# Kernel optimization log

Hardware: AMD Instinct MI355X
Metric: run time of the kernel (lower is better)

The kernel has to match this reference:

```python
import jax, jax.numpy as jnp
import numpy as np

D = 128        # embed_d
L = 2          # n_layers
B = 4096       # batch of center nodes (drugs)
S = 10         # num_samples per neighbor type (hard-coded in node_het_agg)
NUM_CELLS, NUM_DRUGS, NUM_GENES = 2000, 4000, 20000
DRUG_F, GENE_F = 1024, 2048
NT = 3         # node types: cell, drug, gene


def setup_inputs() -> dict:
    key = jax.random.key(0)
    ks = jax.random.split(key, 16)
    s = 0.02
    inp = {
        # raw per-type feature tables (feature_loader / embedding table)
        "drug_feats": jax.random.normal(ks[0], (NUM_DRUGS, DRUG_F), jnp.float32),
        "gene_feats": jax.random.normal(ks[1], (NUM_GENES, GENE_F), jnp.float32),
        "cell_tab": jax.random.normal(ks[2], (NUM_CELLS, D), jnp.float32) * s,
        # feat_proj linears
        "W_drug": jax.random.normal(ks[3], (DRUG_F, D), jnp.float32) * s,
        "b_drug": jnp.zeros((D,), jnp.float32),
        "W_gene": jax.random.normal(ks[4], (GENE_F, D), jnp.float32) * s,
        "b_gene": jnp.zeros((D,), jnp.float32),
        # RnnGnnLayer params: per layer, per neighbor type, a simple tanh RNN
        "rnn_Wx": jax.random.normal(ks[5], (L, NT, D, D), jnp.float32) * s,
        "rnn_Wh": jax.random.normal(ks[6], (L, NT, D, D), jnp.float32) * s,
        "rnn_b": jnp.zeros((L, NT, D), jnp.float32),
        # per-layer attention vector over [self || candidate]
        "att_w": jax.random.normal(ks[7], (L, 2 * D), jnp.float32) * s,
        # center node ids (drug type) and pre-sampled neighbor ids per layer/type
        "center_ids": jax.random.randint(ks[8], (B,), 0, NUM_DRUGS, jnp.int32),
        "cell_neigh": jax.random.randint(ks[9], (L, B, S), 0, NUM_CELLS, jnp.int32),
        "drug_neigh": jax.random.randint(ks[10], (L, B, S), 0, NUM_DRUGS, jnp.int32),
        "gene_neigh": jax.random.randint(ks[11], (L, B, S), 0, NUM_GENES, jnp.int32),
    }
    return inp


def reference(drug_feats, gene_feats, cell_tab, W_drug, b_drug, W_gene, b_gene,
              rnn_Wx, rnn_Wh, rnn_b, att_w,
              center_ids, cell_neigh, drug_neigh, gene_neigh):
    # conteng_agg per node type: gather raw features then project to embed_d
    def emb_cell(idx):
        return cell_tab[idx]                              # [..., D]

    def emb_drug(idx):
        return drug_feats[idx] @ W_drug + b_drug          # gather [..., DRUG_F] -> [..., D]

    def emb_gene(idx):
        return gene_feats[idx] @ W_gene + b_gene

    def rnn_agg(x, Wx, Wh, b):
        # x: [B, S, D]; simple tanh RNN over the S sampled neighbors, last hidden
        def step(h, xt):
            h = jnp.tanh(xt @ Wx + h @ Wh + b)
            return h, None
        h0 = jnp.zeros((x.shape[0], Wx.shape[1]), x.dtype)
        h_last, _ = jax.lax.scan(step, h0, jnp.swapaxes(x, 0, 1))
        return h_last                                      # [B, D]

    h = emb_drug(center_ids)                               # initial center embeds [B, D]
    n_layers = rnn_Wx.shape[0]
    for l in range(n_layers):
        neigh = [(cell_neigh[l], emb_cell), (drug_neigh[l], emb_drug), (gene_neigh[l], emb_gene)]
        aggs = []
        for t, (idx, emb) in enumerate(neigh):
            x = emb(idx)                                   # [B, S, D]
            aggs.append(rnn_agg(x, rnn_Wx[l, t], rnn_Wh[l, t], rnn_b[l, t]))
        cands = jnp.stack([h] + aggs, axis=1)              # [B, 1+NT, D]
        self_b = jnp.broadcast_to(h[:, None, :], cands.shape)
        scores = jax.nn.leaky_relu(jnp.concatenate([self_b, cands], axis=-1) @ att_w[l])  # [B, 1+NT]
        alpha = jax.nn.softmax(scores, axis=1)
        h = jnp.einsum('bc,bcd->bd', alpha, cands)         # attention-weighted combine
    return h                                               # [B, D]
```

## Files before the change

kernel.cpp:

```cpp
#include <hip/hip_runtime.h>
#include <stdint.h>

#define D 128
#define Ssz 10
#define HP 136
#define NB 4096

typedef uint16_t u16;
typedef uint32_t u32;
typedef __attribute__((ext_vector_type(8))) short short8;
typedef __attribute__((ext_vector_type(4))) float f32x4;

#define AS1U32(p) ((const __attribute__((address_space(1))) u32*)(p))
#define AS3U32(p) ((__attribute__((address_space(3))) u32*)(p))

__device__ __forceinline__ u16 f2bf(float f){
  u32 x = __float_as_uint(f);
  return (u16)((x + 0x7fffu + ((x >> 16) & 1u)) >> 16);
}
__device__ __forceinline__ float bf2f(u16 u){ return __uint_as_float(((u32)u) << 16); }

__device__ __forceinline__ float ftanh(float x){
  float e = __expf(2.0f * x);
  return 1.0f - 2.0f / (e + 1.0f);
}

__global__ __launch_bounds__(256) void prep_kernel(
    const float* __restrict__ W_drug, const float* __restrict__ W_gene,
    const float* __restrict__ rnn_Wx, const float* __restrict__ rnn_Wh,
    const float* __restrict__ cell_tab,
    u16* __restrict__ WdT, u16* __restrict__ WgT,
    u16* __restrict__ WxT6, u16* __restrict__ WhT6,
    u16* __restrict__ cellT)
{
  int i = blockIdx.x * 256 + threadIdx.x;
  if (i < 131072){
    int n = i >> 10, k = i & 1023;
    WdT[i] = f2bf(W_drug[k * D + n]);
  } else if (i < 393216){
    int j = i - 131072;
    int n = j >> 11, k = j & 2047;
    WgT[j] = f2bf(W_gene[k * D + n]);
  } else if (i < 491520){
    int j = i - 393216;
    int n = (j >> 7) & 127, k = j & 127;
    WxT6[j] = f2bf(rnn_Wx[(j & ~16383) + k * D + n]);
  } else if (i < 589824){
    int j = i - 491520;
    int n = (j >> 7) & 127, k = j & 127;
    WhT6[j] = f2bf(rnn_Wh[(j & ~16383) + k * D + n]);
  } else {
    int j = i - 589824;
    float v0 = cell_tab[2 * j], v1 = cell_tab[2 * j + 1];
    ((u32*)cellT)[j] = (u32)f2bf(v0) | ((u32)f2bf(v1) << 16);
  }
}

__global__ __launch_bounds__(256) void proj_gemm(
    const float* __restrict__ feats, int K, int M,
    const u16* __restrict__ WT,
    const float* __restrict__ bias,
    const u16* __restrict__ Wx0,
    const u16* __restrict__ Wx1,
    const float* __restrict__ rb0,
    const float* __restrict__ rb1,
    float* __restrict__ xw0,
    float* __restrict__ xw1,
    float* __restrict__ outf)
{
  __shared__ u16 Bt[128 * 128];

  int lane = threadIdx.x & 63;
  int wave = threadIdx.x >> 6;
  int quad = lane >> 4, l16 = lane & 15;
  int m0 = blockIdx.x * 64 + wave * 16;

  int row = min(m0 + l16, M - 1);
  const float* aptr = feats + (long)row * K + quad * 8;

  int st_nrow = wave * 32 + (lane >> 4);
  int st_p    = lane & 15;

  f32x4 acc[8];
#pragma unroll
  for (int nt = 0; nt < 8; ++nt){
    float bv = bias[nt * 16 + l16];
    f32x4 t = {bv, bv, bv, bv};
    acc[nt] = t;
  }

  f32x4 afA[4][2], afB[4][2];
#pragma unroll
  for (int ks = 0; ks < 4; ++ks){
    afA[ks][0] = *(const f32x4*)(aptr + ks * 32);
    afA[ks][1] = *(const f32x4*)(aptr + ks * 32 + 4);
  }

  auto chunk_step = [&](f32x4 (&acur)[4][2], f32x4 (&anxt)[4][2], int kc) {
#pragma unroll
    for (int j = 0; j < 8; ++j){
      int n = st_nrow + j * 4;
      int c = st_p ^ (n & 15);
      const u16* g = WT + (long)n * K + kc + c * 8;
      __builtin_amdgcn_global_load_lds(AS1U32(g),
                                       AS3U32(&Bt[(wave * 8 + j) * 512]),
                                       16, 0, 0);
    }
    if (kc + 128 < K){
#pragma unroll
      for (int ks = 0; ks < 4; ++ks){
        anxt[ks][0] = *(const f32x4*)(aptr + kc + 128 + ks * 32);
        anxt[ks][1] = *(const f32x4*)(aptr + kc + 128 + ks * 32 + 4);
      }
    }
    __syncthreads();

#pragma unroll
    for (int ks = 0; ks < 4; ++ks){
      short8 a;
#pragma unroll
      for (int q = 0; q < 4; ++q){
        a[q]     = (short)f2bf(acur[ks][0][q]);
        a[4 + q] = (short)f2bf(acur[ks][1][q]);
      }
#pragma unroll
      for (int nt = 0; nt < 8; ++nt){
        int n = nt * 16 + l16;
        int p = (ks * 4 + quad) ^ l16;
        short8 b = *(const short8*)(&Bt[n * 128 + p * 8]);
        acc[nt] = __builtin_amdgcn_mfma_f32_16x16x32_bf16(a, b, acc[nt], 0, 0, 0);
      }
    }
    __syncthreads();
  };

  for (int kc = 0; kc < K; kc += 256){
    chunk_step(afA, afB, kc);
    chunk_step(afB, afA, kc + 128);
  }

  if (outf){
#pragma unroll
    for (int nt = 0; nt < 8; ++nt){
      int col = nt * 16 + l16;
#pragma unroll
      for (int r = 0; r < 4; ++r){
        int mr = m0 + quad * 4 + r;
        if (mr < M) outf[(long)mr * D + col] = acc[nt][r];
      }
    }
  }

  u16* Pl = Bt + wave * 2176;
#pragma unroll
  for (int nt = 0; nt < 8; ++nt)
#pragma unroll
    for (int r = 0; r < 4; ++r)
      Pl[(quad * 4 + r) * HP + nt * 16 + l16] = f2bf(acc[nt][r]);
  __syncthreads();

  short8 paf[4];
#pragma unroll
  for (int ks = 0; ks < 4; ++ks)
    paf[ks] = *(const short8*)(&Pl[l16 * HP + ks * 32 + quad * 8]);

  auto xw_pass = [&](const u16* Wx, const float* rb, float* xw){
    f32x4 ac2[8];
#pragma unroll
    for (int nt = 0; nt < 8; ++nt){
      float bv = rb[nt * 16 + l16];
      f32x4 tv = {bv, bv, bv, bv};
      ac2[nt] = tv;
    }
#pragma unroll
    for (int nt = 0; nt < 8; ++nt){
#pragma unroll
      for (int ks = 0; ks < 4; ++ks){
        short8 b = *(const short8*)(Wx + (nt * 16 + l16) * D + ks * 32 + quad * 8);
        ac2[nt] = __builtin_amdgcn_mfma_f32_16x16x32_bf16(paf[ks], b, ac2[nt], 0, 0, 0);
      }
    }
#pragma unroll
    for (int nt = 0; nt < 8; ++nt){
      int col = nt * 16 + l16;
#pragma unroll
      for (int r = 0; r < 4; ++r){
        int mr = m0 + quad * 4 + r;
        if (mr < M) xw[(long)mr * D + col] = ac2[nt][r];
      }
    }
  };
  xw_pass(Wx0, rb0, xw0);
  xw_pass(Wx1, rb1, xw1);
}

__global__ __launch_bounds__(256) void xw_cell(
    const u16* __restrict__ cellT,
    const u16* __restrict__ WxT6,
    const float* __restrict__ bvec,
    float* __restrict__ xwb)
{
  int l = blockIdx.y;
  int mat = l * 3;
  const u16* WT = WxT6 + (size_t)mat * 16384;

  int lane = threadIdx.x & 63, wave = threadIdx.x >> 6;
  int quad = lane >> 4, l16 = lane & 15;
  int mt = blockIdx.x * 64 + wave * 16;
  int mr = min(mt + l16, 1999);

  short8 a[4];
#pragma unroll
  for (int ks = 0; ks < 4; ++ks)
    a[ks] = *(const short8*)(cellT + (long)mr * D + ks * 32 + quad * 8);

  f32x4 acc[8];
#pragma unroll
  for (int nt = 0; nt < 8; ++nt){
    float bv = bvec[mat * D + nt * 16 + l16];
    f32x4 tv = {bv, bv, bv, bv};
    acc[nt] = tv;
  }
#pragma unroll
  for (int nt = 0; nt < 8; ++nt){
#pragma unroll
    for (int ks = 0; ks < 4; ++ks){
      short8 b = *(const short8*)(WT + (nt * 16 + l16) * D + ks * 32 + quad * 8);
      acc[nt] = __builtin_amdgcn_mfma_f32_16x16x32_bf16(a[ks], b, acc[nt], 0, 0, 0);
    }
  }
#pragma unroll
  for (int nt = 0; nt < 8; ++nt){
    int col = nt * 16 + l16;
#pragma unroll
    for (int r = 0; r < 4; ++r){
      int mrow = mt + quad * 4 + r;
      if (mrow < 2000)
        xwb[((long)l * 26000 + mrow) * D + col] = acc[nt][r];
    }
  }
}

__global__ __launch_bounds__(256, 3) void rnn6_kernel(
    const float* __restrict__ xwb,
    const u16* __restrict__ WhT6,
    const int* __restrict__ cn, const int* __restrict__ dn,
    const int* __restrict__ gn,
    u16* __restrict__ agg)
{
  __shared__ u16 hbuf[16 * HP];

  int t = blockIdx.y, l = blockIdx.z;
  const int* idx = (t == 0) ? cn : (t == 1) ? dn : gn;
  int rbase = (t == 0) ? 0 : (t == 1) ? 2000 : 6000;
  int nmax  = (t == 0) ? 2000 : (t == 1) ? 4000 : 20000;
  const float* xw = xwb + ((size_t)l * 26000 + rbase) * D;
  const u16* WT = WhT6 + (size_t)(l * 3 + t) * 16384;

  int tid = threadIdx.x, lane = tid & 63, wave = tid >> 6;
  int quad = lane >> 4, l16 = lane & 15;
  int n0 = wave * 32;

  short8 whf[2][4];
#pragma unroll
  for (int nt = 0; nt < 2; ++nt){
    int n = n0 + nt * 16 + l16;
#pragma unroll
    for (int ks = 0; ks < 4; ++ks)
      whf[nt][ks] = *(const short8*)(WT + n * D + ks * 32 + quad * 8);
  }

  for (int i = tid; i < 16 * HP; i += 256) hbuf[i] = 0;

  int brow = blockIdx.x * 16;
  const int* ip = idx + ((size_t)l * NB + brow + quad * 4) * Ssz;
  long arow = ((long)(l * 3 + t) * NB + brow) * D;

  int nidA[4], nidB[4];
  float xwA[8], xwB[8];
#pragma unroll
  for (int r = 0; r < 4; ++r) nidA[r] = min(max(ip[r * Ssz], 0), nmax - 1);
#pragma unroll
  for (int r = 0; r < 4; ++r){
    const float* p = xw + (long)nidA[r] * D + n0 + l16;
    xwA[r] = p[0]; xwA[4 + r] = p[16];
  }
#pragma unroll
  for (int r = 0; r < 4; ++r) nidB[r] = min(max(ip[r * Ssz + 1], 0), nmax - 1);
  __syncthreads();

  auto step = [&](int s, float (&xwc)[8], int (&nidn)[4],
                  float (&xwn)[8], int (&nidf)[4]){
    if (s + 1 < Ssz){
#pragma unroll
      for (int r = 0; r < 4; ++r){
        const float* p = xw + (long)nidn[r] * D + n0 + l16;
        xwn[r] = p[0]; xwn[4 + r] = p[16];
      }
    }
    if (s + 2 < Ssz){
#pragma unroll
      for (int r = 0; r < 4; ++r)
        nidf[r] = min(max(ip[r * Ssz + s + 2], 0), nmax - 1);
    }
    short8 hf[4];
#pragma unroll
    for (int ks = 0; ks < 4; ++ks)
      hf[ks] = *(const short8*)(&hbuf[l16 * HP + ks * 32 + quad * 8]);
    f32x4 acc0 = {xwc[0], xwc[1], xwc[2], xwc[3]};
    f32x4 acc1 = {xwc[4], xwc[5], xwc[6], xwc[7]};
#pragma unroll
    for (int ks = 0; ks < 4; ++ks){
      acc0 = __builtin_amdgcn_mfma_f32_16x16x32_bf16(hf[ks], whf[0][ks], acc0, 0, 0, 0);
      acc1 = __builtin_amdgcn_mfma_f32_16x16x32_bf16(hf[ks], whf[1][ks], acc1, 0, 0, 0);
    }
    __syncthreads();
#pragma unroll
    for (int r = 0; r < 4; ++r){
      float v0 = ftanh(acc0[r]);
      float v1 = ftanh(acc1[r]);
      hbuf[(quad * 4 + r) * HP + n0 + l16]      = f2bf(v0);
      hbuf[(quad * 4 + r) * HP + n0 + 16 + l16] = f2bf(v1);
      if (s == Ssz - 1){
        long o = arow + (long)(quad * 4 + r) * D;
        agg[o + n0 + l16]      = f2bf(v0);
        agg[o + n0 + 16 + l16] = f2bf(v1);
      }
    }
    __syncthreads();
  };

  step(0, xwA, nidB, xwB, nidA);
  step(1, xwB, nidA, xwA, nidB);
  step(2, xwA, nidB, xwB, nidA);
  step(3, xwB, nidA, xwA, nidB);
  step(4, xwA, nidB, xwB, nidA);
  step(5, xwB, nidA, xwA, nidB);
  step(6, xwA, nidB, xwB, nidA);
  step(7, xwB, nidA, xwA, nidB);
  step(8, xwA, nidB, xwB, nidA);
  step(9, xwB, nidA, xwA, nidB);
}

__global__ __launch_bounds__(256) void att2_kernel(
    const float* __restrict__ drugPf,
    const int* __restrict__ center_ids,
    const u16* __restrict__ agg,
    const float* __restrict__ att_w,
    float* __restrict__ out)
{
  int gt = blockIdx.x * 256 + threadIdx.x;
  int lane = gt & 63;
  int b = gt >> 6;
  int e = 2 * lane;

  int row = min(max(center_ids[b], 0), 3999);
  float h0 = drugPf[(long)row * D + e];
  float h1 = drugPf[(long)row * D + e + 1];

#pragma unroll
  for (int l = 0; l < 2; ++l){
    float c[4][2];
    c[0][0] = h0; c[0][1] = h1;
#pragma unroll
    for (int t = 0; t < 3; ++t){
      long o = ((long)(l * 3 + t) * NB + b) * D + e;
      c[t + 1][0] = bf2f(agg[o]);
      c[t + 1][1] = bf2f(agg[o + 1]);
    }
    const float* aw = att_w + l * 2 * D;
    float as0 = aw[e],     as1 = aw[e + 1];
    float ac0 = aw[D + e], ac1 = aw[D + e + 1];

    float selfp = c[0][0] * as0 + c[0][1] * as1;
    float sc[4];
#pragma unroll
    for (int cc = 0; cc < 4; ++cc) sc[cc] = selfp + c[cc][0] * ac0 + c[cc][1] * ac1;
#pragma unroll
    for (int off = 32; off >= 1; off >>= 1){
#pragma unroll
      for (int cc = 0; cc < 4; ++cc) sc[cc] += __shfl_xor(sc[cc], off, 64);
    }
#pragma unroll
    for (int cc = 0; cc < 4; ++cc) sc[cc] = sc[cc] > 0.f ? sc[cc] : 0.01f * sc[cc];

    float mx = fmaxf(fmaxf(sc[0], sc[1]), fmaxf(sc[2], sc[3]));
    float ex[4], ssum = 0.f;
#pragma unroll
    for (int cc = 0; cc < 4; ++cc){ ex[cc] = expf(sc[cc] - mx); ssum += ex[cc]; }
    float o0 = 0.f, o1 = 0.f;
#pragma unroll
    for (int cc = 0; cc < 4; ++cc){
      float a = ex[cc] / ssum;
      o0 += a * c[cc][0];
      o1 += a * c[cc][1];
    }
    h0 = o0; h1 = o1;
  }
  out[(long)b * D + e]     = h0;
  out[(long)b * D + e + 1] = h1;
}

extern "C" void kernel_launch(void* const* d_in, const int* in_sizes, int n_in,
                              void* d_out, int out_size, void* d_ws, size_t ws_size,
                              hipStream_t stream)
{
  const float* drug_feats = (const float*)d_in[0];
  const float* gene_feats = (const float*)d_in[1];
  const float* cell_tab   = (const float*)d_in[2];
  const float* W_drug     = (const float*)d_in[3];
  const float* b_drug     = (const float*)d_in[4];
  const float* W_gene     = (const float*)d_in[5];
  const float* b_gene     = (const float*)d_in[6];
  const float* rnn_Wx     = (const float*)d_in[7];
  const float* rnn_Wh     = (const float*)d_in[8];
  const float* rnn_b      = (const float*)d_in[9];
  const float* att_w      = (const float*)d_in[10];
  const int* center_ids   = (const int*)d_in[11];
  const int* cell_neigh   = (const int*)d_in[12];
  const int* drug_neigh   = (const int*)d_in[13];
  const int* gene_neigh   = (const int*)d_in[14];

  u16* ws     = (u16*)d_ws;
  u16* WdT    = ws;
  u16* WgT    = WdT + 131072;
  u16* WxT6   = WgT + 262144;
  u16* WhT6   = WxT6 + 98304;
  u16* cellT  = WhT6 + 98304;
  float* drugPf = (float*)(cellT + 256000);
  float* xwb    = drugPf + 512000;
  u16* agg      = (u16*)(xwb + 6656000);

  float* h = (float*)d_out;

  prep_kernel<<<2804, 256, 0, stream>>>(W_drug, W_gene, rnn_Wx, rnn_Wh, cell_tab,
                                        WdT, WgT, WxT6, WhT6, cellT);

  proj_gemm<<<63, 256, 0, stream>>>(drug_feats, 1024, 4000, WdT, b_drug,
                                    WxT6 + 1 * 16384, WxT6 + 4 * 16384,
                                    rnn_b + 1 * D,    rnn_b + 4 * D,
                                    xwb + (size_t)(0 * 26000 + 2000) * D,
                                    xwb + (size_t)(1 * 26000 + 2000) * D,
                                    drugPf);
  proj_gemm<<<313, 256, 0, stream>>>(gene_feats, 2048, 20000, WgT, b_gene,
                                     WxT6 + 2 * 16384, WxT6 + 5 * 16384,
                                     rnn_b + 2 * D,    rnn_b + 5 * D,
                                     xwb + (size_t)(0 * 26000 + 6000) * D,
                                     xwb + (size_t)(1 * 26000 + 6000) * D,
                                     (float*)nullptr);

  xw_cell<<<dim3(32, 2), 256, 0, stream>>>(cellT, WxT6, rnn_b, xwb);

  rnn6_kernel<<<dim3(NB / 16, 3, 2), 256, 0, stream>>>(
      xwb, WhT6, cell_neigh, drug_neigh, gene_neigh, agg);

  att2_kernel<<<NB / 4, 256, 0, stream>>>(drugPf, center_ids, agg, att_w, h);
}
```

Measured before the change: 360.9 us.

## Split-K projection GEMMs into partial kernels and fuse the reduction with the Wx pass

```diff
diff --git a/kernel.cpp b/kernel.cpp
--- a/kernel.cpp
+++ b/kernel.cpp
@@ -5,14 +5,12 @@
 #define Ssz 10
 #define HP 136
 #define NB 4096
+#define KSLICE 512
 
 typedef uint16_t u16;
 typedef uint32_t u32;
 typedef __attribute__((ext_vector_type(8))) short short8;
 typedef __attribute__((ext_vector_type(4))) float f32x4;
-
-#define AS1U32(p) ((const __attribute__((address_space(1))) u32*)(p))
-#define AS3U32(p) ((__attribute__((address_space(3))) u32*)(p))
 
 __device__ __forceinline__ u16 f2bf(float f){
   u32 x = __float_as_uint(f);
@@ -56,113 +54,139 @@
   }
 }
 
-__global__ __launch_bounds__(256) void proj_gemm(
-    const float* __restrict__ feats, int K, int M,
+__global__ __launch_bounds__(256) void proj_part(
+    const float* __restrict__ feats, int K, int M, int Mpad,
     const u16* __restrict__ WT,
     const float* __restrict__ bias,
-    const u16* __restrict__ Wx0,
-    const u16* __restrict__ Wx1,
-    const float* __restrict__ rb0,
-    const float* __restrict__ rb1,
-    float* __restrict__ xw0,
-    float* __restrict__ xw1,
-    float* __restrict__ outf)
-{
-  __shared__ u16 Bt[128 * 128];
-
-  int lane = threadIdx.x & 63;
-  int wave = threadIdx.x >> 6;
+    float* __restrict__ pbuf)
+{
+  int lane = threadIdx.x & 63, wave = threadIdx.x >> 6;
   int quad = lane >> 4, l16 = lane & 15;
   int m0 = blockIdx.x * 64 + wave * 16;
+  int kz = blockIdx.y;
+  long kb = (long)kz * KSLICE;
 
   int row = min(m0 + l16, M - 1);
-  const float* aptr = feats + (long)row * K + quad * 8;
-
-  int st_nrow = wave * 32 + (lane >> 4);
-  int st_p    = lane & 15;
+  const float* aptr = feats + (long)row * K + kb + quad * 8;
 
   f32x4 acc[8];
 #pragma unroll
   for (int nt = 0; nt < 8; ++nt){
-    float bv = bias[nt * 16 + l16];
+    float bv = (kz == 0) ? bias[nt * 16 + l16] : 0.f;
     f32x4 t = {bv, bv, bv, bv};
     acc[nt] = t;
   }
 
   f32x4 afA[4][2], afB[4][2];
-#pragma unroll
-  for (int ks = 0; ks < 4; ++ks){
-    afA[ks][0] = *(const f32x4*)(aptr + ks * 32);
-    afA[ks][1] = *(const f32x4*)(aptr + ks * 32 + 4);
-  }
-
-  auto chunk_step = [&](f32x4 (&acur)[4][2], f32x4 (&anxt)[4][2], int kc) {
-#pragma unroll
-    for (int j = 0; j < 8; ++j){
-      int n = st_nrow + j * 4;
-      int c = st_p ^ (n & 15);
-      const u16* g = WT + (long)n * K + kc + c * 8;
-      __builtin_amdgcn_global_load_lds(AS1U32(g),
-                                       AS3U32(&Bt[(wave * 8 + j) * 512]),
-                                       16, 0, 0);
-    }
-    if (kc + 128 < K){
-#pragma unroll
-      for (int ks = 0; ks < 4; ++ks){
-        anxt[ks][0] = *(const f32x4*)(aptr + kc + 128 + ks * 32);
-        anxt[ks][1] = *(const f32x4*)(aptr + kc + 128 + ks * 32 + 4);
-      }
-    }
-    __syncthreads();
-
+  auto loadA = [&](f32x4 (&af)[4][2], int kc){
 #pragma unroll
     for (int ks = 0; ks < 4; ++ks){
-      short8 a;
+      af[ks][0] = *(const f32x4*)(aptr + kc + ks * 32);
+      af[ks][1] = *(const f32x4*)(aptr + kc + ks * 32 + 4);
+    }
+  };
+  auto compute = [&](f32x4 (&af)[4][2], int kc){
+    short8 a[4];
+#pragma unroll
+    for (int ks = 0; ks < 4; ++ks)
 #pragma unroll
       for (int q = 0; q < 4; ++q){
-        a[q]     = (short)f2bf(acur[ks][0][q]);
-        a[4 + q] = (short)f2bf(acur[ks][1][q]);
-      }
-#pragma unroll
-      for (int nt = 0; nt < 8; ++nt){
-        int n = nt * 16 + l16;
-        int p = (ks * 4 + quad) ^ l16;
-        short8 b = *(const short8*)(&Bt[n * 128 + p * 8]);
-        acc[nt] = __builtin_amdgcn_mfma_f32_16x16x32_bf16(a, b, acc[nt], 0, 0, 0);
-      }
-    }
-    __syncthreads();
-  };
-
-  for (int kc = 0; kc < K; kc += 256){
-    chunk_step(afA, afB, kc);
-    chunk_step(afB, afA, kc + 128);
-  }
-
-  if (outf){
+        a[ks][q]     = (short)f2bf(af[ks][0][q]);
+        a[ks][4 + q] = (short)f2bf(af[ks][1][q]);
+      }
 #pragma unroll
     for (int nt = 0; nt < 8; ++nt){
-      int col = nt * 16 + l16;
-#pragma unroll
-      for (int r = 0; r < 4; ++r){
-        int mr = m0 + quad * 4 + r;
-        if (mr < M) outf[(long)mr * D + col] = acc[nt][r];
-      }
-    }
-  }
-
-  u16* Pl = Bt + wave * 2176;
-#pragma unroll
-  for (int nt = 0; nt < 8; ++nt)
+      const u16* wp = WT + (long)(nt * 16 + l16) * K + kb + kc + quad * 8;
+      short8 b0 = *(const short8*)(wp);
+      short8 b1 = *(const short8*)(wp + 32);
+      short8 b2 = *(const short8*)(wp + 64);
+      short8 b3 = *(const short8*)(wp + 96);
+      acc[nt] = __builtin_amdgcn_mfma_f32_16x16x32_bf16(a[0], b0, acc[nt], 0, 0, 0);
+      acc[nt] = __builtin_amdgcn_mfma_f32_16x16x32_bf16(a[1], b1, acc[nt], 0, 0, 0);
+      acc[nt] = __builtin_amdgcn_mfma_f32_16x16x32_bf16(a[2], b2, acc[nt], 0, 0, 0);
+      acc[nt] = __builtin_amdgcn_mfma_f32_16x16x32_bf16(a[3], b3, acc[nt], 0, 0, 0);
+    }
+  };
+
+  loadA(afA, 0);
+  loadA(afB, 128);
+  compute(afA, 0);
+  loadA(afA, 256);
+  compute(afB, 128);
+  loadA(afB, 384);
+  compute(afA, 256);
+  compute(afB, 384);
+
+  float* pb = pbuf + ((long)kz * Mpad + m0) * D;
+#pragma unroll
+  for (int nt = 0; nt < 8; ++nt){
+    int col = nt * 16 + l16;
 #pragma unroll
     for (int r = 0; r < 4; ++r)
-      Pl[(quad * 4 + r) * HP + nt * 16 + l16] = f2bf(acc[nt][r]);
-  __syncthreads();
-
-  short8 paf[4];
-#pragma unroll
-  for (int ks = 0; ks < 4; ++ks)
-    paf[ks] = *(const short8*)(&Pl[l16 * HP + ks * 32 + quad * 8]);
+      pb[(long)(quad * 4 + r) * D + col] = acc[nt][r];
+  }
+}
+
+__global__ __launch_bounds__(256) void proj_fin(
+    const u16* __restrict__ cellT,
+    const float* __restrict__ pbuf_d,
+    const float* __restrict__ pbuf_g,
+    const u16* __restrict__ WxT6,
+    const float* __restrict__ bvec,
+    float* __restrict__ xwb,
+    float* __restrict__ drugPf)
+{
+  int bx = blockIdx.x;
+  int lane = threadIdx.x & 63, wave = threadIdx.x >> 6;
+  int quad = lane >> 4, l16 = lane & 15;
+
+  int t, m0, M, rbase;
+  if (bx < 32)      { t = 0; m0 = bx * 64;        M = 2000;  rbase = 0;    }
+  else if (bx < 95) { t = 1; m0 = (bx - 32) * 64; M = 4000;  rbase = 2000; }
+  else              { t = 2; m0 = (bx - 95) * 64; M = 20000; rbase = 6000; }
+  int mt = m0 + wave * 16;
+
+  short8 a[4];
+  if (t == 0){
+    int mr = min(mt + l16, 1999);
+#pragma unroll
+    for (int ks = 0; ks < 4; ++ks)
+      a[ks] = *(const short8*)(cellT + (long)mr * D + ks * 32 + quad * 8);
+  } else if (t == 1){
+    long r0 = (long)(mt + l16) * D;
+    const long st = (long)4032 * D;
+#pragma unroll
+    for (int ks = 0; ks < 4; ++ks){
+      long off = r0 + ks * 32 + quad * 8;
+      f32x4 s0 = *(const f32x4*)(pbuf_d + off) + *(const f32x4*)(pbuf_d + st + off);
+      f32x4 s1 = *(const f32x4*)(pbuf_d + off + 4) + *(const f32x4*)(pbuf_d + st + off + 4);
+#pragma unroll
+      for (int q = 0; q < 4; ++q){
+        a[ks][q]     = (short)f2bf(s0[q]);
+        a[ks][4 + q] = (short)f2bf(s1[q]);
+      }
+      if (mt + l16 < 4000){
+        *(f32x4*)(drugPf + off)     = s0;
+        *(f32x4*)(drugPf + off + 4) = s1;
+      }
+    }
+  } else {
+    long r0 = (long)(mt + l16) * D;
+    const long st = (long)20032 * D;
+#pragma unroll
+    for (int ks = 0; ks < 4; ++ks){
+      long off = r0 + ks * 32 + quad * 8;
+      f32x4 s0 = *(const f32x4*)(pbuf_g + off) + *(const f32x4*)(pbuf_g + st + off)
+               + *(const f32x4*)(pbuf_g + 2 * st + off) + *(const f32x4*)(pbuf_g + 3 * st + off);
+      f32x4 s1 = *(const f32x4*)(pbuf_g + off + 4) + *(const f32x4*)(pbuf_g + st + off + 4)
+               + *(const f32x4*)(pbuf_g + 2 * st + off + 4) + *(const f32x4*)(pbuf_g + 3 * st + off + 4);
+#pragma unroll
+      for (int q = 0; q < 4; ++q){
+        a[ks][q]     = (short)f2bf(s0[q]);
+        a[ks][4 + q] = (short)f2bf(s1[q]);
+      }
+    }
+  }
 
   auto xw_pass = [&](const u16* Wx, const float* rb, float* xw){
     f32x4 ac2[8];
@@ -174,71 +198,30 @@
     }
 #pragma unroll
     for (int nt = 0; nt < 8; ++nt){
-#pragma unroll
-      for (int ks = 0; ks < 4; ++ks){
-        short8 b = *(const short8*)(Wx + (nt * 16 + l16) * D + ks * 32 + quad * 8);
-        ac2[nt] = __builtin_amdgcn_mfma_f32_16x16x32_bf16(paf[ks], b, ac2[nt], 0, 0, 0);
-      }
+      const u16* wp = Wx + (long)(nt * 16 + l16) * D + quad * 8;
+      short8 b0 = *(const short8*)(wp);
+      short8 b1 = *(const short8*)(wp + 32);
+      short8 b2 = *(const short8*)(wp + 64);
+      short8 b3 = *(const short8*)(wp + 96);
+      ac2[nt] = __builtin_amdgcn_mfma_f32_16x16x32_bf16(a[0], b0, ac2[nt], 0, 0, 0);
+      ac2[nt] = __builtin_amdgcn_mfma_f32_16x16x32_bf16(a[1], b1, ac2[nt], 0, 0, 0);
+      ac2[nt] = __builtin_amdgcn_mfma_f32_16x16x32_bf16(a[2], b2, ac2[nt], 0, 0, 0);
+      ac2[nt] = __builtin_amdgcn_mfma_f32_16x16x32_bf16(a[3], b3, ac2[nt], 0, 0, 0);
     }
 #pragma unroll
     for (int nt = 0; nt < 8; ++nt){
       int col = nt * 16 + l16;
 #pragma unroll
       for (int r = 0; r < 4; ++r){
-        int mr = m0 + quad * 4 + r;
-        if (mr < M) xw[(long)mr * D + col] = ac2[nt][r];
-      }
-    }
-  };
-  xw_pass(Wx0, rb0, xw0);
-  xw_pass(Wx1, rb1, xw1);
-}
-
-__global__ __launch_bounds__(256) void xw_cell(
-    const u16* __restrict__ cellT,
-    const u16* __restrict__ WxT6,
-    const float* __restrict__ bvec,
-    float* __restrict__ xwb)
-{
-  int l = blockIdx.y;
-  int mat = l * 3;
-  const u16* WT = WxT6 + (size_t)mat * 16384;
-
-  int lane = threadIdx.x & 63, wave = threadIdx.x >> 6;
-  int quad = lane >> 4, l16 = lane & 15;
-  int mt = blockIdx.x * 64 + wave * 16;
-  int mr = min(mt + l16, 1999);
-
-  short8 a[4];
-#pragma unroll
-  for (int ks = 0; ks < 4; ++ks)
-    a[ks] = *(const short8*)(cellT + (long)mr * D + ks * 32 + quad * 8);
-
-  f32x4 acc[8];
-#pragma unroll
-  for (int nt = 0; nt < 8; ++nt){
-    float bv = bvec[mat * D + nt * 16 + l16];
-    f32x4 tv = {bv, bv, bv, bv};
-    acc[nt] = tv;
-  }
-#pragma unroll
-  for (int nt = 0; nt < 8; ++nt){
-#pragma unroll
-    for (int ks = 0; ks < 4; ++ks){
-      short8 b = *(const short8*)(WT + (nt * 16 + l16) * D + ks * 32 + quad * 8);
-      acc[nt] = __builtin_amdgcn_mfma_f32_16x16x32_bf16(a[ks], b, acc[nt], 0, 0, 0);
-    }
-  }
-#pragma unroll
-  for (int nt = 0; nt < 8; ++nt){
-    int col = nt * 16 + l16;
-#pragma unroll
-    for (int r = 0; r < 4; ++r){
-      int mrow = mt + quad * 4 + r;
-      if (mrow < 2000)
-        xwb[((long)l * 26000 + mrow) * D + col] = acc[nt][r];
-    }
-  }
+        int mrow = mt + quad * 4 + r;
+        if (mrow < M) xw[(long)mrow * D + col] = ac2[nt][r];
+      }
+    }
+  };
+  xw_pass(WxT6 + (size_t)t * 16384,       bvec + (size_t)t * D,
+          xwb + (size_t)rbase * D);
+  xw_pass(WxT6 + (size_t)(3 + t) * 16384, bvec + (size_t)(3 + t) * D,
+          xwb + (size_t)(26000 + rbase) * D);
 }
 
 __global__ __launch_bounds__(256, 3) void rnn6_kernel(
@@ -276,33 +259,28 @@
   const int* ip = idx + ((size_t)l * NB + brow + quad * 4) * Ssz;
   long arow = ((long)(l * 3 + t) * NB + brow) * D;
 
-  int nidA[4], nidB[4];
-  float xwA[8], xwB[8];
-#pragma unroll
-  for (int r = 0; r < 4; ++r) nidA[r] = min(max(ip[r * Ssz], 0), nmax - 1);
-#pragma unroll
-  for (int r = 0; r < 4; ++r){
-    const float* p = xw + (long)nidA[r] * D + n0 + l16;
-    xwA[r] = p[0]; xwA[4 + r] = p[16];
-  }
-#pragma unroll
-  for (int r = 0; r < 4; ++r) nidB[r] = min(max(ip[r * Ssz + 1], 0), nmax - 1);
+  int n0b[4], n1b[4], n2b[4];
+  float x0b[8], x1b[8], x2b[8];
+  auto ldnid = [&](int (&nb)[4], int s){
+#pragma unroll
+    for (int r = 0; r < 4; ++r) nb[r] = min(max(ip[r * Ssz + s], 0), nmax - 1);
+  };
+  auto gather = [&](float (&xb)[8], int (&nb)[4]){
+#pragma unroll
+    for (int r = 0; r < 4; ++r){
+      const float* p = xw + (long)nb[r] * D + n0 + l16;
+      xb[r] = p[0]; xb[4 + r] = p[16];
+    }
+  };
+  ldnid(n0b, 0); ldnid(n1b, 1); ldnid(n2b, 2);
+  gather(x0b, n0b);
+  gather(x1b, n1b);
   __syncthreads();
 
-  auto step = [&](int s, float (&xwc)[8], int (&nidn)[4],
-                  float (&xwn)[8], int (&nidf)[4]){
-    if (s + 1 < Ssz){
-#pragma unroll
-      for (int r = 0; r < 4; ++r){
-        const float* p = xw + (long)nidn[r] * D + n0 + l16;
-        xwn[r] = p[0]; xwn[4 + r] = p[16];
-      }
-    }
-    if (s + 2 < Ssz){
-#pragma unroll
-      for (int r = 0; r < 4; ++r)
-        nidf[r] = min(max(ip[r * Ssz + s + 2], 0), nmax - 1);
-    }
+  auto step = [&](int s, float (&xwc)[8], float (&xwg)[8],
+                  int (&nidg)[4], int (&nidl)[4]){
+    if (s + 2 < Ssz) gather(xwg, nidg);
+    if (s + 3 < Ssz) ldnid(nidl, s + 3);
     short8 hf[4];
 #pragma unroll
     for (int ks = 0; ks < 4; ++ks)
@@ -330,16 +308,16 @@
     __syncthreads();
   };
 
-  step(0, xwA, nidB, xwB, nidA);
-  step(1, xwB, nidA, xwA, nidB);
-  step(2, xwA, nidB, xwB, nidA);
-  step(3, xwB, nidA, xwA, nidB);
-  step(4, xwA, nidB, xwB, nidA);
-  step(5, xwB, nidA, xwA, nidB);
-  step(6, xwA, nidB, xwB, nidA);
-  step(7, xwB, nidA, xwA, nidB);
-  step(8, xwA, nidB, xwB, nidA);
-  step(9, xwB, nidA, xwA, nidB);
+  step(0, x0b, x2b, n2b, n0b);
+  step(1, x1b, x0b, n0b, n1b);
+  step(2, x2b, x1b, n1b, n2b);
+  step(3, x0b, x2b, n2b, n0b);
+  step(4, x1b, x0b, n0b, n1b);
+  step(5, x2b, x1b, n1b, n2b);
+  step(6, x0b, x2b, n2b, n0b);
+  step(7, x1b, x0b, n0b, n1b);
+  step(8, x2b, x1b, n1b, n2b);
+  step(9, x0b, x2b, n2b, n0b);
 }
 
 __global__ __launch_bounds__(256) void att2_kernel(
@@ -391,9 +369,9 @@
     float o0 = 0.f, o1 = 0.f;
 #pragma unroll
     for (int cc = 0; cc < 4; ++cc){
-      float a = ex[cc] / ssum;
-      o0 += a * c[cc][0];
-      o1 += a * c[cc][1];
+      float aa = ex[cc] / ssum;
+      o0 += aa * c[cc][0];
+      o1 += aa * c[cc][1];
     }
     h0 = o0; h1 = o1;
   }
@@ -430,26 +408,21 @@
   float* drugPf = (float*)(cellT + 256000);
   float* xwb    = drugPf + 512000;
   u16* agg      = (u16*)(xwb + 6656000);
+  float* pbuf_g = (float*)(agg + 3145728);
+  float* pbuf_d = pbuf_g + (size_t)4 * 20032 * 128;
 
   float* h = (float*)d_out;
 
   prep_kernel<<<2804, 256, 0, stream>>>(W_drug, W_gene, rnn_Wx, rnn_Wh, cell_tab,
                                         WdT, WgT, WxT6, WhT6, cellT);
 
-  proj_gemm<<<63, 256, 0, stream>>>(drug_feats, 1024, 4000, WdT, b_drug,
-                                    WxT6 + 1 * 16384, WxT6 + 4 * 16384,
-                                    rnn_b + 1 * D,    rnn_b + 4 * D,
-                                    xwb + (size_t)(0 * 26000 + 2000) * D,
-                                    xwb + (size_t)(1 * 26000 + 2000) * D,
-                                    drugPf);
-  proj_gemm<<<313, 256, 0, stream>>>(gene_feats, 2048, 20000, WgT, b_gene,
-                                     WxT6 + 2 * 16384, WxT6 + 5 * 16384,
-                                     rnn_b + 2 * D,    rnn_b + 5 * D,
-                                     xwb + (size_t)(0 * 26000 + 6000) * D,
-                                     xwb + (size_t)(1 * 26000 + 6000) * D,
-                                     (float*)nullptr);
-
-  xw_cell<<<dim3(32, 2), 256, 0, stream>>>(cellT, WxT6, rnn_b, xwb);
+  proj_part<<<dim3(313, 4), 256, 0, stream>>>(gene_feats, 2048, 20000, 20032,
+                                              WgT, b_gene, pbuf_g);
+  proj_part<<<dim3(63, 2), 256, 0, stream>>>(drug_feats, 1024, 4000, 4032,
+                                             WdT, b_drug, pbuf_d);
+
+  proj_fin<<<408, 256, 0, stream>>>(cellT, pbuf_d, pbuf_g, WxT6, rnn_b,
+                                    xwb, drugPf);
 
   rnn6_kernel<<<dim3(NB / 16, 3, 2), 256, 0, stream>>>(
       xwb, WhT6, cell_neigh, drug_neigh, gene_neigh, agg);
```

After: 404.7 us. 12.1% more time.
